# Kernel optimization log

Hardware: AMD Instinct MI355X
Metric: run time of the kernel (lower is better)

## Reference

```python
import jax, jax.numpy as jnp
import numpy as np

B, N, QD, KD, VD, H = 8192, 524288, 128, 128, 128, 256


def setup_inputs() -> dict:
    key = jax.random.key(0)
    ks = jax.random.split(key, 12)
    return {
        "query": jax.random.normal(ks[0], (B, QD), jnp.float32),
        "key": jax.random.normal(ks[1], (N, H), jnp.float32),
        "value": jax.random.normal(ks[2], (N, H), jnp.float32),
        "batch": jnp.sort(jax.random.randint(ks[3], (N,), 0, B)).astype(jnp.int64),
        "Wq": jax.random.normal(ks[4], (KD, QD), jnp.float32) * 0.05,
        "bq": jax.random.normal(ks[5], (KD,), jnp.float32) * 0.05,
        "Wk": jax.random.normal(ks[6], (KD, H), jnp.float32) * 0.05,
        "bk": jax.random.normal(ks[7], (KD,), jnp.float32) * 0.05,
        "Wv": jax.random.normal(ks[8], (VD, H), jnp.float32) * 0.05,
        "bv": jax.random.normal(ks[9], (VD,), jnp.float32) * 0.05,
        "Wo": jax.random.normal(ks[10], (VD, VD), jnp.float32) * 0.05,
        "bo": jax.random.normal(ks[11], (VD,), jnp.float32) * 0.05,
    }


def reference(query, key, value, batch, Wq, bq, Wk, bk, Wv, bv, Wo, bo):
    num_graphs = query.shape[0]
    q = query @ Wq.T + bq          # [B, KD]
    k = key @ Wk.T + bk            # [N, KD]
    v = value @ Wv.T + bv          # [N, VD]
    scale = 1.0 / jnp.sqrt(jnp.asarray(k.shape[-1], k.dtype))
    # per-node score against its graph's query (segment-wise softmax)
    s = jnp.einsum('nk,nk->n', k, q[batch]) * scale        # [N]
    m = jax.ops.segment_max(s, batch, num_segments=num_graphs)
    m = jnp.where(jnp.isfinite(m), m, 0.0)                  # empty segments -> 0
    e = jnp.exp(s - m[batch])                               # [N]
    denom = jax.ops.segment_sum(e, batch, num_segments=num_graphs)          # [B]
    num = jax.ops.segment_sum(e[:, None] * v, batch, num_segments=num_graphs)  # [B, VD]
    out = jnp.where(denom[:, None] > 0, num / jnp.maximum(denom[:, None], 1e-30), 0.0)
    return out @ Wo.T + bo
```

## Files before the change

kernel.cpp:

```cpp
#include <hip/hip_runtime.h>
#include <cmath>


__global__ __launch_bounds__(256) void prep_transpose(
    const float* __restrict__ Wq, const float* __restrict__ Wv,
    const float* __restrict__ Wo, float* __restrict__ WqT,
    float* __restrict__ WvT, float* __restrict__ WoT) {
  int idx = blockIdx.x * 256 + threadIdx.x;
  if (idx < 128 * 128) {
    int d = idx >> 7, j = idx & 127;
    WqT[j * 128 + d] = Wq[idx];
    WoT[j * 128 + d] = Wo[idx];
  }
  if (idx < 128 * 256) {
    int d = idx >> 8, h = idx & 255;
    WvT[h * 128 + d] = Wv[idx];
  }
}

__global__ __launch_bounds__(256) void starts_kernel(
    const int* __restrict__ batch, int N, int B, int* __restrict__ starts) {
  int b = blockIdx.x * 256 + threadIdx.x;
  if (b > B) return;
  int lo = 0, hi = N;
  while (lo < hi) {
    int mid = (lo + hi) >> 1;
    if (batch[mid] < b) lo = mid + 1; else hi = mid;
  }
  starts[b] = lo;
}

__global__ __launch_bounds__(256) void qk_kernel(
    const float* __restrict__ query, const float* __restrict__ WqT,
    const float* __restrict__ bq, const float* __restrict__ Wk,
    const float* __restrict__ bk, float* __restrict__ qk,
    float* __restrict__ cvec, float scale) {
  __shared__ float query_s[8][128];
  __shared__ float q_s[8][128];
  const int t = threadIdx.x;
  const int g0 = blockIdx.x * 8;

#pragma unroll
  for (int k2 = 0; k2 < 4; ++k2) {
    int idx = k2 * 256 + t;
    query_s[idx >> 7][idx & 127] = query[(size_t)g0 * 128 + idx];
  }
  __syncthreads();

  {
    const int d = t & 127;
    const int gb = (t >> 7) * 4;
    float a0 = bq[d], a1 = a0, a2 = a0, a3 = a0;
    for (int j = 0; j < 128; ++j) {
      float w = WqT[j * 128 + d];
      a0 += w * query_s[gb + 0][j];
      a1 += w * query_s[gb + 1][j];
      a2 += w * query_s[gb + 2][j];
      a3 += w * query_s[gb + 3][j];
    }
    q_s[gb + 0][d] = a0; q_s[gb + 1][d] = a1;
    q_s[gb + 2][d] = a2; q_s[gb + 3][d] = a3;
  }
  __syncthreads();

  if (t < 8) {
    float acc = 0.f;
    for (int d = 0; d < 128; ++d) acc += q_s[t][d] * bk[d];
    cvec[g0 + t] = scale * acc;
  }

  {
    float acc[8];
#pragma unroll
    for (int i = 0; i < 8; ++i) acc[i] = 0.f;
    for (int d = 0; d < 128; ++d) {
      float w = Wk[d * 256 + t];
#pragma unroll
      for (int i = 0; i < 8; ++i) acc[i] += w * q_s[i][d];
    }
#pragma unroll
    for (int i = 0; i < 8; ++i) qk[(size_t)(g0 + i) * 256 + t] = scale * acc[i];
  }
}

__global__ __launch_bounds__(256) void attn_main(
    const float* __restrict__ key, const float* __restrict__ value,
    const int* __restrict__ starts, const float* __restrict__ qk,
    const float* __restrict__ cvec, float* __restrict__ vsum,
    float* __restrict__ denom) {
  const int lane = threadIdx.x & 63;
  const int g = blockIdx.x * 4 + (threadIdx.x >> 6);

  const float4 qv = ((const float4*)(qk + (size_t)g * 256))[lane];
  const float cb = cvec[g];
  const int n0 = starts[g], n1 = starts[g + 1];

  float m = -INFINITY;
  float den = 0.f;
  float4 vs = make_float4(0.f, 0.f, 0.f, 0.f);

  for (int n = n0; n < n1; ++n) {
    const float4 kv = ((const float4*)(key + (size_t)n * 256))[lane];
    const float4 vv = ((const float4*)(value + (size_t)n * 256))[lane];
    float p = kv.x * qv.x + kv.y * qv.y + kv.z * qv.z + kv.w * qv.w;
#pragma unroll
    for (int off = 32; off; off >>= 1) p += __shfl_xor(p, off, 64);
    const float s = p + cb;
    if (s <= m) {
      const float e = __expf(s - m);
      den += e;
      vs.x += e * vv.x; vs.y += e * vv.y; vs.z += e * vv.z; vs.w += e * vv.w;
    } else {
      const float al = __expf(m - s);
      den = den * al + 1.f;
      vs.x = vs.x * al + vv.x; vs.y = vs.y * al + vv.y;
      vs.z = vs.z * al + vv.z; vs.w = vs.w * al + vv.w;
      m = s;
    }
  }

  ((float4*)(vsum + (size_t)g * 256))[lane] = vs;
  if (lane == 0) denom[g] = den;
}

__global__ __launch_bounds__(256) void final_kernel(
    const float* __restrict__ vsum, const float* __restrict__ denom,
    const float* __restrict__ WvT, const float* __restrict__ bv,
    const float* __restrict__ WoT, const float* __restrict__ bo,
    float* __restrict__ out) {
  __shared__ float vs_s[8][256];
  __shared__ float avg_s[8][128];
  __shared__ float den_s[8];
  const int t = threadIdx.x;
  const int g0 = blockIdx.x * 8;

#pragma unroll
  for (int k2 = 0; k2 < 8; ++k2) {
    int idx = k2 * 256 + t;
    vs_s[idx >> 8][idx & 255] = vsum[(size_t)g0 * 256 + idx];
  }
  if (t < 8) den_s[t] = denom[g0 + t];
  __syncthreads();

  {
    const int d = t & 127;
    const int gb = (t >> 7) * 4;
    float a0 = 0.f, a1 = 0.f, a2 = 0.f, a3 = 0.f;
    for (int h = 0; h < 256; ++h) {
      float w = WvT[h * 128 + d];
      a0 += w * vs_s[gb + 0][h];
      a1 += w * vs_s[gb + 1][h];
      a2 += w * vs_s[gb + 2][h];
      a3 += w * vs_s[gb + 3][h];
    }
    float bvd = bv[d], dn;
    dn = den_s[gb + 0]; avg_s[gb + 0][d] = dn > 0.f ? a0 / dn + bvd : 0.f;
    dn = den_s[gb + 1]; avg_s[gb + 1][d] = dn > 0.f ? a1 / dn + bvd : 0.f;
    dn = den_s[gb + 2]; avg_s[gb + 2][d] = dn > 0.f ? a2 / dn + bvd : 0.f;
    dn = den_s[gb + 3]; avg_s[gb + 3][d] = dn > 0.f ? a3 / dn + bvd : 0.f;
  }
  __syncthreads();

  {
    const int o = t & 127;
    const int gb = (t >> 7) * 4;
    float b = bo[o];
    float a0 = b, a1 = b, a2 = b, a3 = b;
    for (int d = 0; d < 128; ++d) {
      float w = WoT[d * 128 + o];
      a0 += w * avg_s[gb + 0][d];
      a1 += w * avg_s[gb + 1][d];
      a2 += w * avg_s[gb + 2][d];
      a3 += w * avg_s[gb + 3][d];
    }
    out[(size_t)(g0 + gb + 0) * 128 + o] = a0;
    out[(size_t)(g0 + gb + 1) * 128 + o] = a1;
    out[(size_t)(g0 + gb + 2) * 128 + o] = a2;
    out[(size_t)(g0 + gb + 3) * 128 + o] = a3;
  }
}

extern "C" void kernel_launch(void* const* d_in, const int* in_sizes, int n_in,
                              void* d_out, int out_size, void* d_ws, size_t ws_size,
                              hipStream_t stream) {
  const float* query = (const float*)d_in[0];
  const float* key   = (const float*)d_in[1];
  const float* value = (const float*)d_in[2];
  const int*   batch = (const int*)d_in[3];
  const float* Wq = (const float*)d_in[4];
  const float* bq = (const float*)d_in[5];
  const float* Wk = (const float*)d_in[6];
  const float* bk = (const float*)d_in[7];
  const float* Wv = (const float*)d_in[8];
  const float* bv = (const float*)d_in[9];
  const float* Wo = (const float*)d_in[10];
  const float* bo = (const float*)d_in[11];
  float* out = (float*)d_out;

  const int B = in_sizes[0] / 128;
  const int N = in_sizes[3];
  const float scale = 0.08838834764831845f;

  char* ws = (char*)d_ws;
  size_t off = 0;
  auto take = [&](size_t bytes) {
    char* p = ws + off;
    off = (off + bytes + 255) & ~(size_t)255;
    return p;
  };
  int*   starts = (int*)  take((size_t)(B + 1) * 4);
  float* qk     = (float*)take((size_t)B * 256 * 4);
  float* cvec   = (float*)take((size_t)B * 4);
  float* vsum   = (float*)take((size_t)B * 256 * 4);
  float* denom  = (float*)take((size_t)B * 4);
  float* WqT    = (float*)take((size_t)128 * 128 * 4);
  float* WvT    = (float*)take((size_t)256 * 128 * 4);
  float* WoT    = (float*)take((size_t)128 * 128 * 4);
  (void)ws_size; (void)n_in; (void)out_size;

  hipLaunchKernelGGL(prep_transpose, dim3(128), dim3(256), 0, stream,
                     Wq, Wv, Wo, WqT, WvT, WoT);
  hipLaunchKernelGGL(starts_kernel, dim3((B + 1 + 255) / 256), dim3(256), 0, stream,
                     batch, N, B, starts);
  hipLaunchKernelGGL(qk_kernel, dim3(B / 8), dim3(256), 0, stream,
                     query, WqT, bq, Wk, bk, qk, cvec, scale);
  hipLaunchKernelGGL(attn_main, dim3(B / 4), dim3(256), 0, stream,
                     key, value, starts, qk, cvec, vsum, denom);
  hipLaunchKernelGGL(final_kernel, dim3(B / 8), dim3(256), 0, stream,
                     vsum, denom, WvT, bv, WoT, bo, out);
}
```

Measured before the change: 1.089 ms.

## Unroll attention loop by four with prefetch, batched reductions, nontemporal loads

The per-graph attention loop now handles four nodes per iteration. The next group's key and value rows are loaded into registers before the current group is processed, so memory latency overlaps with compute. The four dot products share one butterfly reduction that packs partial sums across lanes, and the online-softmax update runs once per group with a single rescale. Loads use nontemporal hints because key and value are streamed once. This raises register pressure and adds a scalar tail loop for leftover nodes.

Result: faster. 1.065 ms (-2.2%).

```diff
diff --git a/kernel.cpp b/kernel.cpp
--- a/kernel.cpp
+++ b/kernel.cpp
@@ -1,6 +1,8 @@
 #include <hip/hip_runtime.h>
 #include <cmath>
 
+
+typedef float vf4 __attribute__((ext_vector_type(4)));
 
 __global__ __launch_bounds__(256) void prep_transpose(
     const float* __restrict__ Wq, const float* __restrict__ Wv,
@@ -91,35 +93,99 @@
   const int lane = threadIdx.x & 63;
   const int g = blockIdx.x * 4 + (threadIdx.x >> 6);
 
-  const float4 qv = ((const float4*)(qk + (size_t)g * 256))[lane];
+  const vf4 qv = ((const vf4*)(qk + (size_t)g * 256))[lane];
   const float cb = cvec[g];
   const int n0 = starts[g], n1 = starts[g + 1];
+  const int cnt = n1 - n0;
+  const int nb = cnt >> 2;
 
   float m = -INFINITY;
   float den = 0.f;
-  float4 vs = make_float4(0.f, 0.f, 0.f, 0.f);
-
-  for (int n = n0; n < n1; ++n) {
-    const float4 kv = ((const float4*)(key + (size_t)n * 256))[lane];
-    const float4 vv = ((const float4*)(value + (size_t)n * 256))[lane];
+  vf4 vs = {0.f, 0.f, 0.f, 0.f};
+
+  const vf4* kp = (const vf4*)key + (size_t)n0 * 64 + lane;
+  const vf4* vp = (const vf4*)value + (size_t)n0 * 64 + lane;
+
+  vf4 k0, k1, k2, k3, v0, v1, v2, v3;
+
+  auto process = [&](vf4 a0, vf4 a1, vf4 a2, vf4 a3,
+                     vf4 w0, vf4 w1, vf4 w2, vf4 w3) {
+    float p0 = a0.x * qv.x + a0.y * qv.y + a0.z * qv.z + a0.w * qv.w;
+    float p1 = a1.x * qv.x + a1.y * qv.y + a1.z * qv.z + a1.w * qv.w;
+    float p2 = a2.x * qv.x + a2.y * qv.y + a2.z * qv.z + a2.w * qv.w;
+    float p3 = a3.x * qv.x + a3.y * qv.y + a3.z * qv.z + a3.w * qv.w;
+    const bool b0 = lane & 1;
+    float u0 = (b0 ? p1 : p0) + __shfl_xor(b0 ? p0 : p1, 1, 64);
+    float u1 = (b0 ? p3 : p2) + __shfl_xor(b0 ? p2 : p3, 1, 64);
+    const bool b1 = lane & 2;
+    float x = (b1 ? u1 : u0) + __shfl_xor(b1 ? u0 : u1, 2, 64);
+    x += __shfl_xor(x, 4, 64);
+    x += __shfl_xor(x, 8, 64);
+    x += __shfl_xor(x, 16, 64);
+    x += __shfl_xor(x, 32, 64);
+    const float s0 = __shfl(x, 0, 64) + cb;
+    const float s1 = __shfl(x, 1, 64) + cb;
+    const float s2 = __shfl(x, 2, 64) + cb;
+    const float s3 = __shfl(x, 3, 64) + cb;
+    const float M = fmaxf(fmaxf(fmaxf(s0, s1), fmaxf(s2, s3)), m);
+    const float al = __expf(m - M);
+    const float e0 = __expf(s0 - M);
+    const float e1 = __expf(s1 - M);
+    const float e2 = __expf(s2 - M);
+    const float e3 = __expf(s3 - M);
+    m = M;
+    den = den * al + ((e0 + e1) + (e2 + e3));
+    vs.x = vs.x * al + e0 * w0.x + e1 * w1.x + e2 * w2.x + e3 * w3.x;
+    vs.y = vs.y * al + e0 * w0.y + e1 * w1.y + e2 * w2.y + e3 * w3.y;
+    vs.z = vs.z * al + e0 * w0.z + e1 * w1.z + e2 * w2.z + e3 * w3.z;
+    vs.w = vs.w * al + e0 * w0.w + e1 * w1.w + e2 * w2.w + e3 * w3.w;
+  };
+
+  if (nb > 0) {
+    k0 = __builtin_nontemporal_load(kp);
+    k1 = __builtin_nontemporal_load(kp + 64);
+    k2 = __builtin_nontemporal_load(kp + 128);
+    k3 = __builtin_nontemporal_load(kp + 192);
+    v0 = __builtin_nontemporal_load(vp);
+    v1 = __builtin_nontemporal_load(vp + 64);
+    v2 = __builtin_nontemporal_load(vp + 128);
+    v3 = __builtin_nontemporal_load(vp + 192);
+    for (int b = 0; b + 1 < nb; ++b) {
+      kp += 256; vp += 256;
+      vf4 nk0 = __builtin_nontemporal_load(kp);
+      vf4 nk1 = __builtin_nontemporal_load(kp + 64);
+      vf4 nk2 = __builtin_nontemporal_load(kp + 128);
+      vf4 nk3 = __builtin_nontemporal_load(kp + 192);
+      vf4 nv0 = __builtin_nontemporal_load(vp);
+      vf4 nv1 = __builtin_nontemporal_load(vp + 64);
+      vf4 nv2 = __builtin_nontemporal_load(vp + 128);
+      vf4 nv3 = __builtin_nontemporal_load(vp + 192);
+      process(k0, k1, k2, k3, v0, v1, v2, v3);
+      k0 = nk0; k1 = nk1; k2 = nk2; k3 = nk3;
+      v0 = nv0; v1 = nv1; v2 = nv2; v3 = nv3;
+    }
+    process(k0, k1, k2, k3, v0, v1, v2, v3);
+  }
+
+  for (int n = n0 + (nb << 2); n < n1; ++n) {
+    const vf4 kv = __builtin_nontemporal_load((const vf4*)key + (size_t)n * 64 + lane);
+    const vf4 vv = __builtin_nontemporal_load((const vf4*)value + (size_t)n * 64 + lane);
     float p = kv.x * qv.x + kv.y * qv.y + kv.z * qv.z + kv.w * qv.w;
 #pragma unroll
     for (int off = 32; off; off >>= 1) p += __shfl_xor(p, off, 64);
     const float s = p + cb;
-    if (s <= m) {
-      const float e = __expf(s - m);
-      den += e;
-      vs.x += e * vv.x; vs.y += e * vv.y; vs.z += e * vv.z; vs.w += e * vv.w;
-    } else {
-      const float al = __expf(m - s);
-      den = den * al + 1.f;
-      vs.x = vs.x * al + vv.x; vs.y = vs.y * al + vv.y;
-      vs.z = vs.z * al + vv.z; vs.w = vs.w * al + vv.w;
-      m = s;
-    }
-  }
-
-  ((float4*)(vsum + (size_t)g * 256))[lane] = vs;
+    const float M = fmaxf(m, s);
+    const float al = __expf(m - M);
+    const float e = __expf(s - M);
+    m = M;
+    den = den * al + e;
+    vs.x = vs.x * al + e * vv.x;
+    vs.y = vs.y * al + e * vv.y;
+    vs.z = vs.z * al + e * vv.z;
+    vs.w = vs.w * al + e * vv.w;
+  }
+
+  ((vf4*)(vsum + (size_t)g * 256))[lane] = vs;
   if (lane == 0) denom[g] = den;
 }
 
```
